# Kernel tuning notes

Measured on AMD Instinct MI355X. Metric: run time of the kernel, lower is better.

The kernel has to match this reference:

```python
import jax, jax.numpy as jnp
import numpy as np

PAD_TOKEN_ID = 0
EPS = 1e-12  # torch F.normalize eps

B_Q, L_Q = 64, 32
B_D, L_D = 512, 256
HID, OUT = 768, 128
VOCAB = 30522


def setup_inputs() -> dict:
    key = jax.random.key(0)
    k1, k2, k3, k4, k5 = jax.random.split(key, 5)
    return {
        "q_hidden": jax.random.normal(k1, (B_Q, L_Q, HID), dtype=jnp.float32),
        "d_hidden": jax.random.normal(k2, (B_D, L_D, HID), dtype=jnp.float32),
        "d_input_ids": jax.random.randint(k3, (B_D, L_D), 0, VOCAB, dtype=jnp.int32),
        "skiplist": jax.random.randint(k4, (64,), 0, VOCAB, dtype=jnp.int32),
        "W": jax.random.normal(k5, (OUT, HID), dtype=jnp.float32) * (HID ** -0.5),
    }


def _l2norm(x):
    n = jnp.sqrt(jnp.sum(x * x, axis=-1, keepdims=True))
    return x / jnp.maximum(n, EPS)


def reference(q_hidden, d_hidden, d_input_ids, skiplist, W):
    # query(): linear proj + L2 normalize      (B_q, L_q, F)
    Q = _l2norm(jnp.einsum("blh,fh->blf", q_hidden, W))
    # doc(): linear proj + L2 normalize + mask (B_d, L_d, F)
    D = _l2norm(jnp.einsum("blh,fh->blf", d_hidden, W))
    is_pad = d_input_ids == PAD_TOKEN_ID
    is_punct = jnp.any(d_input_ids[..., None] == skiplist, axis=-1)
    d_mask = (~is_pad) & (~is_punct)                     # (B_d, L_d)
    D = D * d_mask[..., None].astype(D.dtype)
    # forward(): reshape to (B, N, L, F) with B = min(B_q, B_d)
    B = min(q_hidden.shape[0], d_hidden.shape[0])
    Qr = Q.reshape(B, -1, L_Q, OUT)                      # (B, 1, L_q, F)
    Dr = D.reshape(B, -1, L_D, OUT)                      # (B, N_p, L_d, F)
    Mr = d_mask.reshape(B, -1, L_D)                      # (B, N_p, L_d)
    # similarity(): cosine MaxSim, Q @ D^T with broadcast over N_p
    sim = jnp.einsum("bqf,bndf->bnqd", Qr[:, 0], Dr)     # (B, N_p, L_q, L_d)
    sim = jnp.where(Mr[:, :, None, :], sim, -jnp.inf)
    sms = jnp.max(sim, axis=-1).mean(axis=-1)            # (B, N_p)
    return sms
```

## Files before the change

kernel.cpp:

```cpp
#include <hip/hip_runtime.h>
#include <stdint.h>

typedef float  f32x4 __attribute__((ext_vector_type(4)));
typedef short  s16x8 __attribute__((ext_vector_type(8)));
typedef unsigned int u32;
typedef unsigned short u16;
typedef unsigned int u32x2 __attribute__((ext_vector_type(2)));

#define HID 768
#define OUTF 128
#define LQ 32
#define LD 256

__device__ __forceinline__ u32 pk_rna(float lo, float hi) {
    u32 a = __builtin_bit_cast(u32, lo) + 0x8000u;
    u32 b = __builtin_bit_cast(u32, hi) + 0x8000u;
    return __builtin_amdgcn_perm(b, a, 0x07060302u);
}
__device__ __forceinline__ u16 f2bf(float x) {
    return (u16)((__builtin_bit_cast(u32, x) + 0x8000u) >> 16);
}
__device__ __forceinline__ s16x8 cvt8(f32x4 lo, f32x4 hi) {
    union { u32 u[4]; s16x8 v; } ua;
    ua.u[0] = pk_rna(lo[0], lo[1]);
    ua.u[1] = pk_rna(lo[2], lo[3]);
    ua.u[2] = pk_rna(hi[0], hi[1]);
    ua.u[3] = pk_rna(hi[2], hi[3]);
    return ua.v;
}

__global__ __launch_bounds__(256) void wconv(const float* __restrict__ W,
                                             u32* __restrict__ Wb3d) {
    int t = blockIdx.x * 256 + threadIdx.x;
    int j2   = t & 3;
    int lane = (t >> 2) & 63;
    int cf   = (t >> 8) & 7;
    int kk   = t >> 11;
    int l15 = lane & 15, g4 = lane >> 4;
    int f = cf * 16 + l15;
    int k = kk * 32 + g4 * 8 + j2 * 2;
    const float* src = W + (size_t)f * HID + k;
    Wb3d[t] = pk_rna(src[0], src[1]);
}

__global__ __launch_bounds__(256) void qproj(const float* __restrict__ qh,
                                             const u16* __restrict__ Wb3,
                                             u16* __restrict__ Qb) {
    const int b = blockIdx.x;
    const int tid = threadIdx.x;
    const int w = tid >> 6, lane = tid & 63, g = lane >> 4, l15 = lane & 15;

    f32x4 acc[2][2] = {};
    const float* A0 = qh + ((size_t)b * LQ + l15) * HID + g * 8;
    const float* A1 = A0 + 16 * HID;
    const u16* Bp = Wb3 + w * 1024 + lane * 8;

    for (int kk = 0; kk < 24; ++kk) {
        f32x4 x0 = *(const f32x4*)A0;
        f32x4 x1 = *(const f32x4*)(A0 + 4);
        f32x4 y0 = *(const f32x4*)A1;
        f32x4 y1 = *(const f32x4*)(A1 + 4);
        s16x8 b0 = *(const s16x8*)(Bp);
        s16x8 b1 = *(const s16x8*)(Bp + 512);
        s16x8 a0 = cvt8(x0, x1);
        s16x8 a1 = cvt8(y0, y1);
        acc[0][0] = __builtin_amdgcn_mfma_f32_16x16x32_bf16(a0, b0, acc[0][0], 0, 0, 0);
        acc[0][1] = __builtin_amdgcn_mfma_f32_16x16x32_bf16(a0, b1, acc[0][1], 0, 0, 0);
        acc[1][0] = __builtin_amdgcn_mfma_f32_16x16x32_bf16(a1, b0, acc[1][0], 0, 0, 0);
        acc[1][1] = __builtin_amdgcn_mfma_f32_16x16x32_bf16(a1, b1, acc[1][1], 0, 0, 0);
        A0 += 32; A1 += 32; Bp += 4096;
    }

    __shared__ float part[4][32];
    __shared__ float invl[32];
#pragma unroll
    for (int rf = 0; rf < 2; ++rf)
#pragma unroll
        for (int reg = 0; reg < 4; ++reg) {
            float ss = acc[rf][0][reg] * acc[rf][0][reg] + acc[rf][1][reg] * acc[rf][1][reg];
            ss += __shfl_xor(ss, 1); ss += __shfl_xor(ss, 2);
            ss += __shfl_xor(ss, 4); ss += __shfl_xor(ss, 8);
            if (l15 == 0) part[w][rf * 16 + g * 4 + reg] = ss;
        }
    __syncthreads();
    if (tid < 32) {
        float ss = part[0][tid] + part[1][tid] + part[2][tid] + part[3][tid];
        invl[tid] = 1.f / fmaxf(sqrtf(ss), 1e-12f);
    }
    __syncthreads();
#pragma unroll
    for (int rf = 0; rf < 2; ++rf)
#pragma unroll
        for (int cf = 0; cf < 2; ++cf)
#pragma unroll
            for (int reg = 0; reg < 4; ++reg) {
                int q = rf * 16 + g * 4 + reg;
                int f = w * 32 + cf * 16 + l15;
                Qb[(size_t)b * LQ * OUTF + q * OUTF + f] = f2bf(acc[rf][cf][reg] * invl[q]);
            }
}

__global__ __launch_bounds__(512, 2) void dmax(const float* __restrict__ dh,
                                               const int* __restrict__ ids,
                                               const int* __restrict__ skiplist,
                                               const u16* __restrict__ Wb3,
                                               const u16* __restrict__ Qb,
                                               float* __restrict__ out) {
    const int bid = blockIdx.x;
    const int tid = threadIdx.x;
    const int w = tid >> 6, lane = tid & 63, g4 = lane >> 4, l15 = lane & 15;
    const int qh_ = w >> 2;

    __shared__ __align__(16) u16 stg[2][12288];
    __shared__ __align__(16) u16 outb[2][2048];
    __shared__ float nrm[2][8][16];
    __shared__ float wsum[8];
    __shared__ int ms[512];
    __shared__ int sk[64];

    const int va = tid, vb = tid + 512, vc = tid + 1024,
              vd = tid + 1536, ve = tid + 2048, vf = tid + 2560;
#define LADOF(v) (((v) / 192) * 1536 + (((((v) % 192)) * 8) ^ ((((v) / 192) & 7) << 4)))
    const int lad0 = LADOF(va), lad1 = LADOF(vb), lad2 = LADOF(vc),
              lad3 = LADOF(vd), lad4 = LADOF(ve), lad5 = LADOF(vf);

    const int swz = (l15 & 7) << 4, sw45 = swz & 48, sw6 = swz & 64;
    const int aoffE = l15 * 1536 + ((g4 * 16) ^ sw45) + sw6;
    const int aoffO = l15 * 1536 + ((g4 * 16) ^ sw45) + 64 - sw6;
    const int doffE = l15 * 256 + ((g4 * 16) ^ sw45) + sw6;
    const int doffO = l15 * 256 + ((g4 * 16) ^ sw45) + 64 - sw6;

    f32x4 LA0, LA1, LA2, LA3, LA4, LA5, LB0, LB1, LB2, LB3, LB4, LB5;
    s16x8 Qr0, Qr1, Qr2, Qr3;
    float rmaxH[4] = {-INFINITY, -INFINITY, -INFINITY, -INFINITY};

#define SLABBASE(sab) ((const char*)dh + (size_t)(bid + (((sab) >> 4) << 8)) * 786432 \
                       + (size_t)((sab) & 15) * 49152)

#define LISSUE(sab, S) { const char* gb_ = SLABBASE(sab); \
    S##0 = *(const f32x4*)(gb_ + va * 16); S##1 = *(const f32x4*)(gb_ + vb * 16); \
    S##2 = *(const f32x4*)(gb_ + vc * 16); S##3 = *(const f32x4*)(gb_ + vd * 16); \
    S##4 = *(const f32x4*)(gb_ + ve * 16); S##5 = *(const f32x4*)(gb_ + vf * 16); }

#define WSTORE(P, S) { char* sb_ = (char*)&stg[P][0]; u32x2 p_; \
    p_[0] = pk_rna(S##0[0], S##0[1]); p_[1] = pk_rna(S##0[2], S##0[3]); *(u32x2*)(sb_ + lad0) = p_; \
    p_[0] = pk_rna(S##1[0], S##1[1]); p_[1] = pk_rna(S##1[2], S##1[3]); *(u32x2*)(sb_ + lad1) = p_; \
    p_[0] = pk_rna(S##2[0], S##2[1]); p_[1] = pk_rna(S##2[2], S##2[3]); *(u32x2*)(sb_ + lad2) = p_; \
    p_[0] = pk_rna(S##3[0], S##3[1]); p_[1] = pk_rna(S##3[2], S##3[3]); *(u32x2*)(sb_ + lad3) = p_; \
    p_[0] = pk_rna(S##4[0], S##4[1]); p_[1] = pk_rna(S##4[2], S##4[3]); *(u32x2*)(sb_ + lad4) = p_; \
    p_[0] = pk_rna(S##5[0], S##5[1]); p_[1] = pk_rna(S##5[2], S##5[3]); *(u32x2*)(sb_ + lad5) = p_; }

#define QLOAD(doc_) { const u16* qp_ = Qb + (size_t)((bid + (doc_) * 256) >> 3) * 4096 \
                      + (qh_ * 16 + l15) * 128 + g4 * 8; \
    Qr0 = *(const s16x8*)(qp_);      Qr1 = *(const s16x8*)(qp_ + 32); \
    Qr2 = *(const s16x8*)(qp_ + 64); Qr3 = *(const s16x8*)(qp_ + 96); }

#define GEMMN(P) { \
    const char* Ab_ = (const char*)&stg[P][0]; \
    f32x4 ac0_ = {}, ac1_ = {}; \
    _Pragma("unroll") for (int kkp = 0; kkp < 12; ++kkp) { \
        s16x8 ae_ = *(const s16x8*)(Ab_ + aoffE + kkp * 128); \
        s16x8 ao_ = *(const s16x8*)(Ab_ + aoffO + kkp * 128); \
        ac0_ = __builtin_amdgcn_mfma_f32_16x16x32_bf16(ae_, Bf[2 * kkp],     ac0_, 0, 0, 0); \
        ac1_ = __builtin_amdgcn_mfma_f32_16x16x32_bf16(ao_, Bf[2 * kkp + 1], ac1_, 0, 0, 0); \
    } \
    f32x4 aG_ = ac0_ + ac1_; \
    _Pragma("unroll") for (int rg = 0; rg < 4; ++rg) { \
        float ss_ = aG_[rg] * aG_[rg]; \
        ss_ += __shfl_xor(ss_, 1); ss_ += __shfl_xor(ss_, 2); \
        ss_ += __shfl_xor(ss_, 4); ss_ += __shfl_xor(ss_, 8); \
        if (l15 == 0) nrm[P][w][g4 * 4 + rg] = ss_; \
        int dr_ = g4 * 4 + rg; \
        int of_ = (dr_ * 256 + (w * 16 + l15) * 2) ^ ((dr_ & 7) << 4); \
        *(u16*)((char*)&outb[P][0] + of_) = f2bf(aG_[rg]); \
    } }

#define TAIL(P, sb) { \
    const char* Db_ = (const char*)&outb[P][0]; \
    s16x8 d0_ = *(const s16x8*)(Db_ + doffE); \
    s16x8 d1_ = *(const s16x8*)(Db_ + doffO); \
    s16x8 d2_ = *(const s16x8*)(Db_ + doffE + 128); \
    s16x8 d3_ = *(const s16x8*)(Db_ + doffO + 128); \
    f32x4 s2_ = {}; \
    s2_ = __builtin_amdgcn_mfma_f32_16x16x32_bf16(Qr0, d0_, s2_, 0, 0, 0); \
    s2_ = __builtin_amdgcn_mfma_f32_16x16x32_bf16(Qr1, d1_, s2_, 0, 0, 0); \
    s2_ = __builtin_amdgcn_mfma_f32_16x16x32_bf16(Qr2, d2_, s2_, 0, 0, 0); \
    s2_ = __builtin_amdgcn_mfma_f32_16x16x32_bf16(Qr3, d3_, s2_, 0, 0, 0); \
    float ssv_ = nrm[P][0][l15] + nrm[P][1][l15] + nrm[P][2][l15] + nrm[P][3][l15] \
               + nrm[P][4][l15] + nrm[P][5][l15] + nrm[P][6][l15] + nrm[P][7][l15]; \
    float inv_ = 1.f / fmaxf(sqrtf(ssv_), 1e-12f); \
    int keep_ = ms[(((sb) >> 4) << 8) + (((sb) & 15) << 4) + l15]; \
    _Pragma("unroll") for (int rg = 0; rg < 4; ++rg) { \
        float v_ = keep_ ? s2_[rg] * inv_ : -INFINITY; \
        rmaxH[rg] = fmaxf(rmaxH[rg], v_); } \
    if (((sb) & 15) == 15) { \
        float ps_ = 0.f; \
        _Pragma("unroll") for (int rg = 0; rg < 4; ++rg) { \
            float v_ = rmaxH[rg]; \
            v_ = fmaxf(v_, __shfl_xor(v_, 1)); v_ = fmaxf(v_, __shfl_xor(v_, 2)); \
            v_ = fmaxf(v_, __shfl_xor(v_, 4)); v_ = fmaxf(v_, __shfl_xor(v_, 8)); \
            ps_ += v_; rmaxH[rg] = -INFINITY; } \
        ps_ += __shfl_xor(ps_, 16); ps_ += __shfl_xor(ps_, 32); \
        if (lane == 0) wsum[w] = ps_; \
        asm volatile("s_waitcnt lgkmcnt(0)" ::: "memory"); \
        __builtin_amdgcn_s_barrier(); \
        if (tid == 0) out[bid + (((sb) >> 4) << 8)] = (wsum[0] + wsum[4]) * (1.f / 32.f); \
        if ((sb) == 15) { QLOAD(1); } \
    } }

    LISSUE(0, LA);
    LISSUE(1, LB);

    s16x8 Bf[24];
#pragma unroll
    for (int kk = 0; kk < 24; ++kk)
        Bf[kk] = *(const s16x8*)(Wb3 + (size_t)(kk * 8 + w) * 512 + lane * 8);

    if (tid < 64) sk[tid] = skiplist[tid];
    asm volatile("s_waitcnt lgkmcnt(0)" ::: "memory");
    __builtin_amdgcn_s_barrier();
    {
        int d_ = tid >> 8, r_ = tid & 255;
        int id_ = ids[(size_t)(bid + d_ * 256) * 256 + r_];
        int keep_ = (id_ != 0);
#pragma unroll
        for (int j = 0; j < 64; ++j) keep_ &= (id_ != sk[j]);
        ms[tid] = keep_;
    }
    WSTORE(0, LA);
    QLOAD(0);
    asm volatile("s_waitcnt lgkmcnt(0)" ::: "memory");
    __builtin_amdgcn_s_barrier();

    for (int it = 0; it < 16; ++it) {
        const int sbE = 2 * it, sbO = 2 * it + 1;

        if (sbE + 2 < 32) LISSUE(sbE + 2, LA);
        WSTORE(1, LB);
        GEMMN(0);
        asm volatile("s_waitcnt lgkmcnt(0)" ::: "memory");
        __builtin_amdgcn_s_barrier();
        TAIL(0, sbE);

        if (sbO + 2 < 32) LISSUE(sbO + 2, LB);
        if (sbO + 1 < 32) WSTORE(0, LA);
        GEMMN(1);
        asm volatile("s_waitcnt lgkmcnt(0)" ::: "memory");
        __builtin_amdgcn_s_barrier();
        TAIL(1, sbO);
    }
}

extern "C" void kernel_launch(void* const* d_in, const int* in_sizes, int n_in,
                              void* d_out, int out_size, void* d_ws, size_t ws_size,
                              hipStream_t stream) {
    const float* q_hidden = (const float*)d_in[0];
    const float* d_hidden = (const float*)d_in[1];
    const int*   d_ids    = (const int*)d_in[2];
    const int*   skiplist = (const int*)d_in[3];
    const float* W        = (const float*)d_in[4];
    float* out = (float*)d_out;

    u16* Wb3 = (u16*)d_ws;
    u16* Qb  = (u16*)((char*)d_ws + 256 * 1024);

    wconv<<<192, 256, 0, stream>>>(W, (u32*)Wb3);
    qproj<<<64, 256, 0, stream>>>(q_hidden, Wb3, Qb);
    dmax<<<256, 512, 0, stream>>>(d_hidden, d_ids, skiplist, Wb3, Qb, out);
}
```

Baseline: 104.8 us.

## Triple-buffer doc slab staging, widen loads, and skip redundant tail MaxSim waves

Raises the global-to-LDS prefetch depth from two to three slabs, using a third LDS stage buffer and a third register set, so more HBM latency is hidden behind the projection GEMM. Each thread now loads 32 contiguous bytes and writes 16-byte packed bf16 stores to LDS instead of 8-byte ones. The norm buffer is transposed so the tail can read the eight partial sums with two vector loads. Only one wave per query half now runs the redundant Q·D MFMA tail and its reduction. In exchange, register pressure rises under launch_bounds(512,2) with the existing 24-fragment weight cache, which risks spills, and the larger LDS footprint may limit occupancy.

```diff
diff --git a/kernel.cpp b/kernel.cpp
--- a/kernel.cpp
+++ b/kernel.cpp
@@ -5,7 +5,7 @@
 typedef short  s16x8 __attribute__((ext_vector_type(8)));
 typedef unsigned int u32;
 typedef unsigned short u16;
-typedef unsigned int u32x2 __attribute__((ext_vector_type(2)));
+typedef unsigned int u32x4 __attribute__((ext_vector_type(4)));
 
 #define HID 768
 #define OUTF 128
@@ -111,18 +111,15 @@
     const int w = tid >> 6, lane = tid & 63, g4 = lane >> 4, l15 = lane & 15;
     const int qh_ = w >> 2;
 
-    __shared__ __align__(16) u16 stg[2][12288];
+    __shared__ __align__(16) u16 stg[3][12288];
     __shared__ __align__(16) u16 outb[2][2048];
-    __shared__ float nrm[2][8][16];
+    __shared__ __align__(16) float nrm[2][16][8];
     __shared__ float wsum[8];
     __shared__ int ms[512];
     __shared__ int sk[64];
 
-    const int va = tid, vb = tid + 512, vc = tid + 1024,
-              vd = tid + 1536, ve = tid + 2048, vf = tid + 2560;
-#define LADOF(v) (((v) / 192) * 1536 + (((((v) % 192)) * 8) ^ ((((v) / 192) & 7) << 4)))
-    const int lad0 = LADOF(va), lad1 = LADOF(vb), lad2 = LADOF(vc),
-              lad3 = LADOF(vd), lad4 = LADOF(ve), lad5 = LADOF(vf);
+#define PADOF(v) (((v) / 192) * 1536 + (((((v) % 192)) * 8) ^ ((((v) / 192) & 7) << 4)))
+    const int pad0 = PADOF(2 * tid), pad1 = PADOF(2 * tid + 1024), pad2 = PADOF(2 * tid + 2048);
 
     const int swz = (l15 & 7) << 4, sw45 = swz & 48, sw6 = swz & 64;
     const int aoffE = l15 * 1536 + ((g4 * 16) ^ sw45) + sw6;
@@ -130,33 +127,38 @@
     const int doffE = l15 * 256 + ((g4 * 16) ^ sw45) + sw6;
     const int doffO = l15 * 256 + ((g4 * 16) ^ sw45) + 64 - sw6;
 
-    f32x4 LA0, LA1, LA2, LA3, LA4, LA5, LB0, LB1, LB2, LB3, LB4, LB5;
+    f32x4 LA0, LA1, LA2, LA3, LA4, LA5, LB0, LB1, LB2, LB3, LB4, LB5,
+          LC0, LC1, LC2, LC3, LC4, LC5;
     s16x8 Qr0, Qr1, Qr2, Qr3;
     float rmaxH[4] = {-INFINITY, -INFINITY, -INFINITY, -INFINITY};
 
 #define SLABBASE(sab) ((const char*)dh + (size_t)(bid + (((sab) >> 4) << 8)) * 786432 \
                        + (size_t)((sab) & 15) * 49152)
 
-#define LISSUE(sab, S) { const char* gb_ = SLABBASE(sab); \
-    S##0 = *(const f32x4*)(gb_ + va * 16); S##1 = *(const f32x4*)(gb_ + vb * 16); \
-    S##2 = *(const f32x4*)(gb_ + vc * 16); S##3 = *(const f32x4*)(gb_ + vd * 16); \
-    S##4 = *(const f32x4*)(gb_ + ve * 16); S##5 = *(const f32x4*)(gb_ + vf * 16); }
-
-#define WSTORE(P, S) { char* sb_ = (char*)&stg[P][0]; u32x2 p_; \
-    p_[0] = pk_rna(S##0[0], S##0[1]); p_[1] = pk_rna(S##0[2], S##0[3]); *(u32x2*)(sb_ + lad0) = p_; \
-    p_[0] = pk_rna(S##1[0], S##1[1]); p_[1] = pk_rna(S##1[2], S##1[3]); *(u32x2*)(sb_ + lad1) = p_; \
-    p_[0] = pk_rna(S##2[0], S##2[1]); p_[1] = pk_rna(S##2[2], S##2[3]); *(u32x2*)(sb_ + lad2) = p_; \
-    p_[0] = pk_rna(S##3[0], S##3[1]); p_[1] = pk_rna(S##3[2], S##3[3]); *(u32x2*)(sb_ + lad3) = p_; \
-    p_[0] = pk_rna(S##4[0], S##4[1]); p_[1] = pk_rna(S##4[2], S##4[3]); *(u32x2*)(sb_ + lad4) = p_; \
-    p_[0] = pk_rna(S##5[0], S##5[1]); p_[1] = pk_rna(S##5[2], S##5[3]); *(u32x2*)(sb_ + lad5) = p_; }
+#define LISSUE(sab, S) { const char* gb_ = SLABBASE(sab) + 32 * tid; \
+    S##0 = *(const f32x4*)(gb_);          S##1 = *(const f32x4*)(gb_ + 16); \
+    S##2 = *(const f32x4*)(gb_ + 16384);  S##3 = *(const f32x4*)(gb_ + 16400); \
+    S##4 = *(const f32x4*)(gb_ + 32768);  S##5 = *(const f32x4*)(gb_ + 32784); }
+
+#define WSTORE(P, S) { char* sb_ = (char*)&stg[P][0]; u32x4 q_; \
+    q_[0] = pk_rna(S##0[0], S##0[1]); q_[1] = pk_rna(S##0[2], S##0[3]); \
+    q_[2] = pk_rna(S##1[0], S##1[1]); q_[3] = pk_rna(S##1[2], S##1[3]); \
+    *(u32x4*)(sb_ + pad0) = q_; \
+    q_[0] = pk_rna(S##2[0], S##2[1]); q_[1] = pk_rna(S##2[2], S##2[3]); \
+    q_[2] = pk_rna(S##3[0], S##3[1]); q_[3] = pk_rna(S##3[2], S##3[3]); \
+    *(u32x4*)(sb_ + pad1) = q_; \
+    q_[0] = pk_rna(S##4[0], S##4[1]); q_[1] = pk_rna(S##4[2], S##4[3]); \
+    q_[2] = pk_rna(S##5[0], S##5[1]); q_[3] = pk_rna(S##5[2], S##5[3]); \
+    *(u32x4*)(sb_ + pad2) = q_; }
 
 #define QLOAD(doc_) { const u16* qp_ = Qb + (size_t)((bid + (doc_) * 256) >> 3) * 4096 \
                       + (qh_ * 16 + l15) * 128 + g4 * 8; \
     Qr0 = *(const s16x8*)(qp_);      Qr1 = *(const s16x8*)(qp_ + 32); \
     Qr2 = *(const s16x8*)(qp_ + 64); Qr3 = *(const s16x8*)(qp_ + 96); }
 
-#define GEMMN(P) { \
+#define GEMMN(P, s_) { \
     const char* Ab_ = (const char*)&stg[P][0]; \
+    u16* ob_ = &outb[(s_) & 1][0]; \
     f32x4 ac0_ = {}, ac1_ = {}; \
     _Pragma("unroll") for (int kkp = 0; kkp < 12; ++kkp) { \
         s16x8 ae_ = *(const s16x8*)(Ab_ + aoffE + kkp * 128); \
@@ -169,47 +171,62 @@
         float ss_ = aG_[rg] * aG_[rg]; \
         ss_ += __shfl_xor(ss_, 1); ss_ += __shfl_xor(ss_, 2); \
         ss_ += __shfl_xor(ss_, 4); ss_ += __shfl_xor(ss_, 8); \
-        if (l15 == 0) nrm[P][w][g4 * 4 + rg] = ss_; \
+        if (l15 == 0) nrm[(s_) & 1][g4 * 4 + rg][w] = ss_; \
         int dr_ = g4 * 4 + rg; \
         int of_ = (dr_ * 256 + (w * 16 + l15) * 2) ^ ((dr_ & 7) << 4); \
-        *(u16*)((char*)&outb[P][0] + of_) = f2bf(aG_[rg]); \
+        *(u16*)((char*)ob_ + of_) = f2bf(aG_[rg]); \
     } }
 
-#define TAIL(P, sb) { \
-    const char* Db_ = (const char*)&outb[P][0]; \
-    s16x8 d0_ = *(const s16x8*)(Db_ + doffE); \
-    s16x8 d1_ = *(const s16x8*)(Db_ + doffO); \
-    s16x8 d2_ = *(const s16x8*)(Db_ + doffE + 128); \
-    s16x8 d3_ = *(const s16x8*)(Db_ + doffO + 128); \
-    f32x4 s2_ = {}; \
-    s2_ = __builtin_amdgcn_mfma_f32_16x16x32_bf16(Qr0, d0_, s2_, 0, 0, 0); \
-    s2_ = __builtin_amdgcn_mfma_f32_16x16x32_bf16(Qr1, d1_, s2_, 0, 0, 0); \
-    s2_ = __builtin_amdgcn_mfma_f32_16x16x32_bf16(Qr2, d2_, s2_, 0, 0, 0); \
-    s2_ = __builtin_amdgcn_mfma_f32_16x16x32_bf16(Qr3, d3_, s2_, 0, 0, 0); \
-    float ssv_ = nrm[P][0][l15] + nrm[P][1][l15] + nrm[P][2][l15] + nrm[P][3][l15] \
-               + nrm[P][4][l15] + nrm[P][5][l15] + nrm[P][6][l15] + nrm[P][7][l15]; \
-    float inv_ = 1.f / fmaxf(sqrtf(ssv_), 1e-12f); \
-    int keep_ = ms[(((sb) >> 4) << 8) + (((sb) & 15) << 4) + l15]; \
-    _Pragma("unroll") for (int rg = 0; rg < 4; ++rg) { \
-        float v_ = keep_ ? s2_[rg] * inv_ : -INFINITY; \
-        rmaxH[rg] = fmaxf(rmaxH[rg], v_); } \
+#define TAIL(sb) { \
+    if ((w & 3) == 0) { \
+        const char* Db_ = (const char*)&outb[(sb) & 1][0]; \
+        s16x8 d0_ = *(const s16x8*)(Db_ + doffE); \
+        s16x8 d1_ = *(const s16x8*)(Db_ + doffO); \
+        s16x8 d2_ = *(const s16x8*)(Db_ + doffE + 128); \
+        s16x8 d3_ = *(const s16x8*)(Db_ + doffO + 128); \
+        f32x4 s2_ = {}; \
+        s2_ = __builtin_amdgcn_mfma_f32_16x16x32_bf16(Qr0, d0_, s2_, 0, 0, 0); \
+        s2_ = __builtin_amdgcn_mfma_f32_16x16x32_bf16(Qr1, d1_, s2_, 0, 0, 0); \
+        s2_ = __builtin_amdgcn_mfma_f32_16x16x32_bf16(Qr2, d2_, s2_, 0, 0, 0); \
+        s2_ = __builtin_amdgcn_mfma_f32_16x16x32_bf16(Qr3, d3_, s2_, 0, 0, 0); \
+        f32x4 n0_ = *(const f32x4*)&nrm[(sb) & 1][l15][0]; \
+        f32x4 n1_ = *(const f32x4*)&nrm[(sb) & 1][l15][4]; \
+        float ssv_ = (n0_[0] + n0_[1] + n0_[2] + n0_[3]) \
+                   + (n1_[0] + n1_[1] + n1_[2] + n1_[3]); \
+        float inv_ = 1.f / fmaxf(sqrtf(ssv_), 1e-12f); \
+        int keep_ = ms[(((sb) >> 4) << 8) + (((sb) & 15) << 4) + l15]; \
+        _Pragma("unroll") for (int rg = 0; rg < 4; ++rg) { \
+            float v_ = keep_ ? s2_[rg] * inv_ : -INFINITY; \
+            rmaxH[rg] = fmaxf(rmaxH[rg], v_); } \
+    } \
     if (((sb) & 15) == 15) { \
-        float ps_ = 0.f; \
-        _Pragma("unroll") for (int rg = 0; rg < 4; ++rg) { \
-            float v_ = rmaxH[rg]; \
-            v_ = fmaxf(v_, __shfl_xor(v_, 1)); v_ = fmaxf(v_, __shfl_xor(v_, 2)); \
-            v_ = fmaxf(v_, __shfl_xor(v_, 4)); v_ = fmaxf(v_, __shfl_xor(v_, 8)); \
-            ps_ += v_; rmaxH[rg] = -INFINITY; } \
-        ps_ += __shfl_xor(ps_, 16); ps_ += __shfl_xor(ps_, 32); \
-        if (lane == 0) wsum[w] = ps_; \
+        if ((w & 3) == 0) { \
+            float ps_ = 0.f; \
+            _Pragma("unroll") for (int rg = 0; rg < 4; ++rg) { \
+                float v_ = rmaxH[rg]; \
+                v_ = fmaxf(v_, __shfl_xor(v_, 1)); v_ = fmaxf(v_, __shfl_xor(v_, 2)); \
+                v_ = fmaxf(v_, __shfl_xor(v_, 4)); v_ = fmaxf(v_, __shfl_xor(v_, 8)); \
+                ps_ += v_; rmaxH[rg] = -INFINITY; } \
+            ps_ += __shfl_xor(ps_, 16); ps_ += __shfl_xor(ps_, 32); \
+            if (lane == 0) wsum[w] = ps_; \
+            if ((sb) == 15) { QLOAD(1); } \
+        } \
         asm volatile("s_waitcnt lgkmcnt(0)" ::: "memory"); \
         __builtin_amdgcn_s_barrier(); \
         if (tid == 0) out[bid + (((sb) >> 4) << 8)] = (wsum[0] + wsum[4]) * (1.f / 32.f); \
-        if ((sb) == 15) { QLOAD(1); } \
     } }
+
+#define SLABSTEP(s_, PG_, PW_, RN_, RW_, doIssue_, doWr_) { \
+    if (doIssue_) LISSUE((s_) + 3, RN_); \
+    if (doWr_) WSTORE(PW_, RW_); \
+    GEMMN(PG_, s_); \
+    asm volatile("s_waitcnt lgkmcnt(0)" ::: "memory"); \
+    __builtin_amdgcn_s_barrier(); \
+    TAIL(s_); }
 
     LISSUE(0, LA);
     LISSUE(1, LB);
+    LISSUE(2, LC);
 
     s16x8 Bf[24];
 #pragma unroll
@@ -228,27 +245,18 @@
         ms[tid] = keep_;
     }
     WSTORE(0, LA);
-    QLOAD(0);
+    if ((w & 3) == 0) { QLOAD(0); }
     asm volatile("s_waitcnt lgkmcnt(0)" ::: "memory");
     __builtin_amdgcn_s_barrier();
 
-    for (int it = 0; it < 16; ++it) {
-        const int sbE = 2 * it, sbO = 2 * it + 1;
-
-        if (sbE + 2 < 32) LISSUE(sbE + 2, LA);
-        WSTORE(1, LB);
-        GEMMN(0);
-        asm volatile("s_waitcnt lgkmcnt(0)" ::: "memory");
-        __builtin_amdgcn_s_barrier();
-        TAIL(0, sbE);
-
-        if (sbO + 2 < 32) LISSUE(sbO + 2, LB);
-        if (sbO + 1 < 32) WSTORE(0, LA);
-        GEMMN(1);
-        asm volatile("s_waitcnt lgkmcnt(0)" ::: "memory");
-        __builtin_amdgcn_s_barrier();
-        TAIL(1, sbO);
-    }
+    for (int j = 0; j < 10; ++j) {
+        const int s0 = 3 * j;
+        SLABSTEP(s0,     0, 1, LA, LB, true,        true);
+        SLABSTEP(s0 + 1, 1, 2, LB, LC, true,        true);
+        SLABSTEP(s0 + 2, 2, 0, LC, LA, s0 + 5 < 32, true);
+    }
+    SLABSTEP(30, 0, 1, LA, LB, false, true);
+    SLABSTEP(31, 1, 2, LB, LC, false, false);
 }
 
 extern "C" void kernel_launch(void* const* d_in, const int* in_sizes, int n_in,
```

New measurement: 103.2 us. About the same (-1.5%).
